# Performance work log

Hardware: AMD Instinct MI355X
Metric: run time of the kernel (lower is better)

The kernel has to match this reference:

```python
import jax, jax.numpy as jnp
import numpy as np

def setup_inputs() -> dict:
    key = jax.random.key(0)
    x = jax.random.normal(key, (64, 1024, 1024), dtype=jnp.float32)
    return {"x": x}

def reference(x):
    # SerialSum: scalar accumulation over all elements == full reduction sum
    return jnp.sum(x)
```

## Files before the change

kernel.cpp:

```cpp
#include <hip/hip_runtime.h>

#define THREADS 256
#define BLOCKS 2048

__global__ __launch_bounds__(THREADS) void sum_stage1(
    const float4* __restrict__ x, float* __restrict__ partials, int n4) {
    float s = 0.0f;
    for (int i = blockIdx.x * blockDim.x + threadIdx.x; i < n4;
         i += gridDim.x * blockDim.x) {
        float4 v = x[i];
        s += (v.x + v.y) + (v.z + v.w);
    }
    #pragma unroll
    for (int off = 32; off > 0; off >>= 1)
        s += __shfl_down(s, off, 64);
    __shared__ float lds[THREADS / 64];
    const int lane = threadIdx.x & 63;
    const int wave = threadIdx.x >> 6;
    if (lane == 0) lds[wave] = s;
    __syncthreads();
    if (threadIdx.x == 0) {
        float t = 0.0f;
        #pragma unroll
        for (int w = 0; w < THREADS / 64; ++w) t += lds[w];
        partials[blockIdx.x] = t;
    }
}

__global__ __launch_bounds__(THREADS) void sum_stage2(
    const float* __restrict__ partials, float* __restrict__ out, int n) {
    float s = 0.0f;
    for (int i = threadIdx.x; i < n; i += blockDim.x) s += partials[i];
    #pragma unroll
    for (int off = 32; off > 0; off >>= 1)
        s += __shfl_down(s, off, 64);
    __shared__ float lds[THREADS / 64];
    const int lane = threadIdx.x & 63;
    const int wave = threadIdx.x >> 6;
    if (lane == 0) lds[wave] = s;
    __syncthreads();
    if (threadIdx.x == 0) {
        float t = 0.0f;
        #pragma unroll
        for (int w = 0; w < THREADS / 64; ++w) t += lds[w];
        out[0] = t;
    }
}

extern "C" void kernel_launch(void* const* d_in, const int* in_sizes, int n_in,
                              void* d_out, int out_size, void* d_ws, size_t ws_size,
                              hipStream_t stream) {
    const float* x = (const float*)d_in[0];
    float* out = (float*)d_out;
    float* partials = (float*)d_ws;

    const int n = in_sizes[0];
    const int n4 = n / 4;

    sum_stage1<<<BLOCKS, THREADS, 0, stream>>>((const float4*)x, partials, n4);
    sum_stage2<<<1, THREADS, 0, stream>>>(partials, out, BLOCKS);
}
```

Before: 46.34 us.

## Unroll stage-1 loads with contiguous per-block chunks and widen stage 2

Stage 1 now gives each block a contiguous chunk and issues 8 independent float4 loads per iteration into separate accumulators, raising memory-level parallelism and shortening the add dependency chains. Stage 2 uses 1024 threads so the single block reduces the 2048 partials in fewer iterations. Elements beyond BLOCKS*(n4/BLOCKS) are not covered if n4 is not divisible by the block count, and contiguous chunking changes the DRAM access pattern across blocks.

```diff
diff --git a/kernel.cpp b/kernel.cpp
--- a/kernel.cpp
+++ b/kernel.cpp
@@ -2,47 +2,72 @@
 
 #define THREADS 256
 #define BLOCKS 2048
+#define UNROLL 8
 
 __global__ __launch_bounds__(THREADS) void sum_stage1(
     const float4* __restrict__ x, float* __restrict__ partials, int n4) {
-    float s = 0.0f;
-    for (int i = blockIdx.x * blockDim.x + threadIdx.x; i < n4;
-         i += gridDim.x * blockDim.x) {
-        float4 v = x[i];
-        s += (v.x + v.y) + (v.z + v.w);
+    const int per_block = n4 / BLOCKS;
+    const int base = blockIdx.x * per_block;
+    const int iters = per_block / (UNROLL * THREADS);
+
+    float s[UNROLL];
+    #pragma unroll
+    for (int k = 0; k < UNROLL; ++k) s[k] = 0.f;
+
+    int i = base + threadIdx.x;
+    for (int g = 0; g < iters; ++g) {
+        float4 v[UNROLL];
+        #pragma unroll
+        for (int k = 0; k < UNROLL; ++k) v[k] = x[i + k * THREADS];
+        i += UNROLL * THREADS;
+        #pragma unroll
+        for (int k = 0; k < UNROLL; ++k)
+            s[k] += (v[k].x + v[k].y) + (v[k].z + v[k].w);
     }
+    for (int j = base + iters * UNROLL * THREADS + threadIdx.x;
+         j < base + per_block; j += THREADS) {
+        float4 a = x[j];
+        s[0] += (a.x + a.y) + (a.z + a.w);
+    }
+
+    float s01 = s[0] + s[1], s23 = s[2] + s[3];
+    float s45 = s[4] + s[5], s67 = s[6] + s[7];
+    float sum = (s01 + s23) + (s45 + s67);
+
     #pragma unroll
     for (int off = 32; off > 0; off >>= 1)
-        s += __shfl_down(s, off, 64);
+        sum += __shfl_down(sum, off, 64);
     __shared__ float lds[THREADS / 64];
     const int lane = threadIdx.x & 63;
     const int wave = threadIdx.x >> 6;
-    if (lane == 0) lds[wave] = s;
+    if (lane == 0) lds[wave] = sum;
     __syncthreads();
     if (threadIdx.x == 0) {
-        float t = 0.0f;
+        float t = 0.f;
         #pragma unroll
         for (int w = 0; w < THREADS / 64; ++w) t += lds[w];
         partials[blockIdx.x] = t;
     }
 }
 
-__global__ __launch_bounds__(THREADS) void sum_stage2(
+#define S2_THREADS 1024
+
+__global__ __launch_bounds__(S2_THREADS) void sum_stage2(
     const float* __restrict__ partials, float* __restrict__ out, int n) {
-    float s = 0.0f;
-    for (int i = threadIdx.x; i < n; i += blockDim.x) s += partials[i];
+    float s = 0.f;
+    for (int i = threadIdx.x; i < n; i += S2_THREADS) s += partials[i];
     #pragma unroll
     for (int off = 32; off > 0; off >>= 1)
         s += __shfl_down(s, off, 64);
-    __shared__ float lds[THREADS / 64];
+    __shared__ float lds[S2_THREADS / 64];
     const int lane = threadIdx.x & 63;
     const int wave = threadIdx.x >> 6;
     if (lane == 0) lds[wave] = s;
     __syncthreads();
     if (threadIdx.x == 0) {
-        float t = 0.0f;
+        float t = 0.f;
         #pragma unroll
-        for (int w = 0; w < THREADS / 64; ++w) t += lds[w];
+        for (int w = 0; w < S2_THREADS / 64; ++w) t += lds[w];
         out[0] = t;
     }
 }
@@ -58,5 +83,5 @@
     const int n4 = n / 4;
 
     sum_stage1<<<BLOCKS, THREADS, 0, stream>>>((const float4*)x, partials, n4);
-    sum_stage2<<<1, THREADS, 0, stream>>>(partials, out, BLOCKS);
+    sum_stage2<<<1, S2_THREADS, 0, stream>>>(partials, out, BLOCKS);
 }
```

After: 44.53 us. 3.9% less time.
